# Kernel optimization log

Hardware: AMD Instinct MI355X
Metric: run time of the kernel (lower is better)

The kernel has to match this reference:

```python
import jax, jax.numpy as jnp
import numpy as np

N_NODES = 100000
N_EDGES = 3200000
FEAT = 64  # pos(32) + vel(32)
OUT_DIM = 2


def setup_inputs() -> dict:
    key = jax.random.key(0)
    k1, k2, k3, k4, k5, k6, k7, k8 = jax.random.split(key, 8)
    pos = jax.random.normal(k1, (N_NODES, 32), dtype=jnp.float32)
    vel = jax.random.normal(k2, (N_NODES, 32), dtype=jnp.float32)
    edge_index = jax.random.randint(k3, (2, N_EDGES), 0, N_NODES, dtype=jnp.int64 if jax.config.jax_enable_x64 else jnp.int32)
    s = 1.0 / np.sqrt(FEAT)
    W_rel = jax.random.uniform(k4, (FEAT, FEAT), jnp.float32, -s, s)
    b_rel = jax.random.uniform(k5, (FEAT,), jnp.float32, -s, s)
    W_root = jax.random.uniform(k6, (FEAT, FEAT), jnp.float32, -s, s)
    W_pred = jax.random.uniform(k7, (FEAT, OUT_DIM), jnp.float32, -s, s)
    b_pred = jax.random.uniform(k8, (OUT_DIM,), jnp.float32, -s, s)
    return {"pos": pos, "vel": vel, "edge_index": edge_index,
            "W_rel": W_rel, "b_rel": b_rel, "W_root": W_root,
            "W_pred": W_pred, "b_pred": b_pred}


def reference(pos, vel, edge_index, W_rel, b_rel, W_root, W_pred, b_pred):
    # h = cat([pos, vel], -1)  -> [N, 64]
    h = jnp.concatenate([pos, vel], axis=-1)
    src, dst = edge_index[0], edge_index[1]
    # GraphConv (PyG, aggr='add'): out_i = lin_rel(sum_{j->i} h_j) + lin_root(h_i)
    msgs = h[src]  # [E, 64] irregular gather
    agg = jax.ops.segment_sum(msgs, dst, num_segments=N_NODES)  # [N, 64]
    conv_out = agg @ W_rel + b_rel + h @ W_root
    # lin_pred
    return conv_out @ W_pred + b_pred
```

## Files before the change

### kernel.cpp

```cpp
#include <hip/hip_runtime.h>

#define N_NODES 100000
#define N_EDGES 3200000
#define FEAT 64
#define OUT_DIM 2

#define SHIFT 8
#define S_NODES 256
#define K_BUCKETS 391
#define CAP 8704
#define NB 256
#define EPB (N_EDGES / NB)


__global__ void fold_weights_kernel(const float* __restrict__ W_rel,
                                    const float* __restrict__ b_rel,
                                    const float* __restrict__ W_root,
                                    const float* __restrict__ W_pred,
                                    const float* __restrict__ b_pred,
                                    float* __restrict__ M,
                                    int* __restrict__ gcount) {
    int t = threadIdx.x;
    if (t < 128) {
        int k = t >> 1, o = t & 1;
        float acc = 0.f;
        #pragma unroll
        for (int f = 0; f < FEAT; ++f) acc += W_rel[k * FEAT + f] * W_pred[f * OUT_DIM + o];
        M[t] = acc;
    } else {
        int tt = t - 128;
        int k = tt >> 1, o = tt & 1;
        float acc = 0.f;
        #pragma unroll
        for (int f = 0; f < FEAT; ++f) acc += W_root[k * FEAT + f] * W_pred[f * OUT_DIM + o];
        M[128 + tt] = acc;
    }
    if (t < OUT_DIM) {
        float acc = b_pred[t];
        #pragma unroll
        for (int f = 0; f < FEAT; ++f) acc += b_rel[f] * W_pred[f * OUT_DIM + t];
        M[256 + t] = acc;
    }
    for (int i = t; i < K_BUCKETS; i += 256) gcount[i] = 0;
}

__global__ __launch_bounds__(256) void node_kernel(const float* __restrict__ pos,
                                                   const float* __restrict__ vel,
                                                   const float* __restrict__ M,
                                                   float* __restrict__ y,
                                                   float* __restrict__ out) {
    __shared__ float sM[258];
    for (int i = threadIdx.x; i < 258; i += 256) sM[i] = M[i];
    __syncthreads();

    int n = blockIdx.x * 256 + threadIdx.x;
    if (n >= N_NODES) return;

    const float4* p4 = (const float4*)(pos + (size_t)n * 32);
    const float4* v4 = (const float4*)(vel + (size_t)n * 32);
    float h[FEAT];
    #pragma unroll
    for (int i = 0; i < 8; ++i) {
        float4 a = p4[i];
        h[i * 4 + 0] = a.x; h[i * 4 + 1] = a.y; h[i * 4 + 2] = a.z; h[i * 4 + 3] = a.w;
    }
    #pragma unroll
    for (int i = 0; i < 8; ++i) {
        float4 a = v4[i];
        h[32 + i * 4 + 0] = a.x; h[32 + i * 4 + 1] = a.y; h[32 + i * 4 + 2] = a.z; h[32 + i * 4 + 3] = a.w;
    }

    float rel0 = 0.f, rel1 = 0.f, ro0 = 0.f, ro1 = 0.f;
    #pragma unroll
    for (int k = 0; k < FEAT; ++k) {
        float hk = h[k];
        rel0 += hk * sM[2 * k + 0];
        rel1 += hk * sM[128 + 2 * k + 0];
        rel1 = rel1;
        rel1 += 0.f;
        ro0 += 0.f;
        ro1 += 0.f;
        (void)0;
        rel1 -= sM[128 + 2 * k + 0] * hk;
        break;
    }
    rel0 = 0.f; rel1 = 0.f; ro0 = 0.f; ro1 = 0.f;
    #pragma unroll
    for (int k = 0; k < FEAT; ++k) {
        float hk = h[k];
        rel0 += hk * sM[2 * k + 0];
        rel1 += hk * sM[2 * k + 1];
        ro0  += hk * sM[128 + 2 * k + 0];
        ro1  += hk * sM[128 + 2 * k + 1];
    }
    ((float2*)y)[n]   = make_float2(rel0, rel1);
    ((float2*)out)[n] = make_float2(ro0 + sM[256], ro1 + sM[257]);
}

__global__ __launch_bounds__(256) void binscatter_kernel(const int* __restrict__ edges,
                                                         int* __restrict__ gcount,
                                                         unsigned* __restrict__ scat) {
    __shared__ int hist[K_BUCKETS];
    __shared__ int cur[K_BUCKETS];
    for (int i = threadIdx.x; i < K_BUCKETS; i += 256) hist[i] = 0;
    __syncthreads();

    const int4* d4 = (const int4*)(edges + N_EDGES) + blockIdx.x * (EPB / 4);
    for (int i = threadIdx.x; i < EPB / 4; i += 256) {
        int4 d = d4[i];
        atomicAdd(&hist[d.x >> SHIFT], 1);
        atomicAdd(&hist[d.y >> SHIFT], 1);
        atomicAdd(&hist[d.z >> SHIFT], 1);
        atomicAdd(&hist[d.w >> SHIFT], 1);
    }
    __syncthreads();

    for (int i = threadIdx.x; i < K_BUCKETS; i += 256)
        cur[i] = atomicAdd(&gcount[i], hist[i]);
    __syncthreads();

    const int4* s4 = (const int4*)(edges + blockIdx.x * EPB);
    for (int i = threadIdx.x; i < EPB / 4; i += 256) {
        int4 s = s4[i];
        int4 d = d4[i];
        int k, p;
        k = d.x >> SHIFT; p = atomicAdd(&cur[k], 1);
        if (p < CAP) scat[(size_t)k * CAP + p] = (unsigned)s.x | ((unsigned)(d.x & (S_NODES - 1)) << 17);
        k = d.y >> SHIFT; p = atomicAdd(&cur[k], 1);
        if (p < CAP) scat[(size_t)k * CAP + p] = (unsigned)s.y | ((unsigned)(d.y & (S_NODES - 1)) << 17);
        k = d.z >> SHIFT; p = atomicAdd(&cur[k], 1);
        if (p < CAP) scat[(size_t)k * CAP + p] = (unsigned)s.z | ((unsigned)(d.z & (S_NODES - 1)) << 17);
        k = d.w >> SHIFT; p = atomicAdd(&cur[k], 1);
        if (p < CAP) scat[(size_t)k * CAP + p] = (unsigned)s.w | ((unsigned)(d.w & (S_NODES - 1)) << 17);
    }
}

__global__ __launch_bounds__(256) void accum_kernel(const unsigned* __restrict__ scat,
                                                    const int* __restrict__ gcount,
                                                    const float* __restrict__ y,
                                                    float* __restrict__ out) {
    __shared__ float acc[S_NODES * 2];
    int t = threadIdx.x;
    acc[t] = 0.f;
    acc[t + S_NODES] = 0.f;
    __syncthreads();

    int k = blockIdx.x;
    int c = gcount[k];
    if (c > CAP) c = CAP;
    const unsigned* sl = scat + (size_t)k * CAP;
    const float2* y2 = (const float2*)y;
    for (int i = t; i < c; i += 256) {
        unsigned p = sl[i];
        int src = p & 0x1FFFF;
        int dl = p >> 17;
        float2 v = y2[src];
        atomicAdd(&acc[dl], v.x);
        atomicAdd(&acc[S_NODES + dl], v.y);
    }
    __syncthreads();

    int node = k * S_NODES + t;
    if (node < N_NODES) {
        float2* o2 = (float2*)out;
        float2 cv = o2[node];
        cv.x += acc[t];
        cv.y += acc[S_NODES + t];
        o2[node] = cv;
    }
}

extern "C" void kernel_launch(void* const* d_in, const int* in_sizes, int n_in,
                              void* d_out, int out_size, void* d_ws, size_t ws_size,
                              hipStream_t stream) {
    const float* pos    = (const float*)d_in[0];
    const float* vel    = (const float*)d_in[1];
    const int*   edges  = (const int*)d_in[2];
    const float* W_rel  = (const float*)d_in[3];
    const float* b_rel  = (const float*)d_in[4];
    const float* W_root = (const float*)d_in[5];
    const float* W_pred = (const float*)d_in[6];
    const float* b_pred = (const float*)d_in[7];
    float* out = (float*)d_out;

    char* ws = (char*)d_ws;
    float*    M      = (float*)ws;
    float*    y      = (float*)(ws + 2048);
    int*      gcount = (int*)(ws + 802048);
    unsigned* scat   = (unsigned*)(ws + 803712);

    fold_weights_kernel<<<1, 256, 0, stream>>>(W_rel, b_rel, W_root, W_pred, b_pred, M, gcount);

    int node_blocks = (N_NODES + 255) / 256;
    node_kernel<<<node_blocks, 256, 0, stream>>>(pos, vel, M, y, out);

    binscatter_kernel<<<NB, 256, 0, stream>>>(edges, gcount, scat);

    accum_kernel<<<K_BUCKETS, 256, 0, stream>>>(scat, gcount, y, out);
}
```

Baseline: 172.8 us.

## Fuse weight folding, node projection and edge binning into one launch

Merges the weight-fold, node projection and bucket-scatter kernels into a single launch. Block ranges split the work: the first 800 blocks bin edges and the remaining blocks fold weights into shared memory and project nodes, so the two phases can overlap and launch gaps disappear. Weight folding is now recomputed by every node block, and gcount is zeroed with a memset. The scatter uses more blocks, skips global atomics for empty buckets, and the accumulation kernel uses 1024 threads with two loads in flight per iteration, at the cost of more shared-atomic contention per block.

```diff
diff --git a/kernel.cpp b/kernel.cpp
--- a/kernel.cpp
+++ b/kernel.cpp
@@ -9,140 +9,117 @@
 #define S_NODES 256
 #define K_BUCKETS 391
 #define CAP 8704
-#define NB 256
+#define NB 800
 #define EPB (N_EDGES / NB)
+#define NODE_BLOCKS 391
 
 
-__global__ void fold_weights_kernel(const float* __restrict__ W_rel,
-                                    const float* __restrict__ b_rel,
-                                    const float* __restrict__ W_root,
-                                    const float* __restrict__ W_pred,
-                                    const float* __restrict__ b_pred,
-                                    float* __restrict__ M,
-                                    int* __restrict__ gcount) {
+__global__ __launch_bounds__(256) void fused_kernel(
+    const float* __restrict__ pos, const float* __restrict__ vel,
+    const int* __restrict__ edges,
+    const float* __restrict__ W_rel, const float* __restrict__ b_rel,
+    const float* __restrict__ W_root, const float* __restrict__ W_pred,
+    const float* __restrict__ b_pred,
+    int* __restrict__ gcount, unsigned* __restrict__ scat,
+    float* __restrict__ y, float* __restrict__ out)
+{
     int t = threadIdx.x;
-    if (t < 128) {
-        int k = t >> 1, o = t & 1;
-        float acc = 0.f;
+    if (blockIdx.x < NB) {
+        __shared__ int hist[K_BUCKETS];
+        __shared__ int cur[K_BUCKETS];
+        for (int i = t; i < K_BUCKETS; i += 256) hist[i] = 0;
+        __syncthreads();
+
+        const int4* d4 = (const int4*)(edges + N_EDGES) + blockIdx.x * (EPB / 4);
+        for (int i = t; i < EPB / 4; i += 256) {
+            int4 d = d4[i];
+            atomicAdd(&hist[d.x >> SHIFT], 1);
+            atomicAdd(&hist[d.y >> SHIFT], 1);
+            atomicAdd(&hist[d.z >> SHIFT], 1);
+            atomicAdd(&hist[d.w >> SHIFT], 1);
+        }
+        __syncthreads();
+
+        for (int i = t; i < K_BUCKETS; i += 256) {
+            int h = hist[i];
+            cur[i] = h ? atomicAdd(&gcount[i], h) : 0;
+        }
+        __syncthreads();
+
+        const int4* s4 = (const int4*)(edges) + blockIdx.x * (EPB / 4);
+        for (int i = t; i < EPB / 4; i += 256) {
+            int4 s = s4[i];
+            int4 d = d4[i];
+            int k, p;
+            k = d.x >> SHIFT; p = atomicAdd(&cur[k], 1);
+            if (p < CAP) scat[(size_t)k * CAP + p] = (unsigned)s.x | ((unsigned)(d.x & (S_NODES - 1)) << 17);
+            k = d.y >> SHIFT; p = atomicAdd(&cur[k], 1);
+            if (p < CAP) scat[(size_t)k * CAP + p] = (unsigned)s.y | ((unsigned)(d.y & (S_NODES - 1)) << 17);
+            k = d.z >> SHIFT; p = atomicAdd(&cur[k], 1);
+            if (p < CAP) scat[(size_t)k * CAP + p] = (unsigned)s.z | ((unsigned)(d.z & (S_NODES - 1)) << 17);
+            k = d.w >> SHIFT; p = atomicAdd(&cur[k], 1);
+            if (p < CAP) scat[(size_t)k * CAP + p] = (unsigned)s.w | ((unsigned)(d.w & (S_NODES - 1)) << 17);
+        }
+    } else {
+        __shared__ float sM[258];
+        if (t < 128) {
+            int k = t >> 1, o = t & 1;
+            float acc = 0.f;
+            #pragma unroll
+            for (int f = 0; f < FEAT; ++f) acc += W_rel[k * FEAT + f] * W_pred[f * OUT_DIM + o];
+            sM[t] = acc;
+        } else {
+            int tt = t - 128;
+            int k = tt >> 1, o = tt & 1;
+            float acc = 0.f;
+            #pragma unroll
+            for (int f = 0; f < FEAT; ++f) acc += W_root[k * FEAT + f] * W_pred[f * OUT_DIM + o];
+            sM[128 + tt] = acc;
+        }
+        if (t < OUT_DIM) {
+            float acc = b_pred[t];
+            #pragma unroll
+            for (int f = 0; f < FEAT; ++f) acc += b_rel[f] * W_pred[f * OUT_DIM + t];
+            sM[256 + t] = acc;
+        }
+        __syncthreads();
+
+        int n = (blockIdx.x - NB) * 256 + t;
+        if (n >= N_NODES) return;
+
+        const float4* p4 = (const float4*)(pos + (size_t)n * 32);
+        const float4* v4 = (const float4*)(vel + (size_t)n * 32);
+        float rel0 = 0.f, rel1 = 0.f, ro0 = 0.f, ro1 = 0.f;
         #pragma unroll
-        for (int f = 0; f < FEAT; ++f) acc += W_rel[k * FEAT + f] * W_pred[f * OUT_DIM + o];
-        M[t] = acc;
-    } else {
-        int tt = t - 128;
-        int k = tt >> 1, o = tt & 1;
-        float acc = 0.f;
+        for (int i = 0; i < 8; ++i) {
+            float4 a = p4[i];
+            int k0 = i * 4;
+            rel0 += a.x * sM[2*k0+0] + a.y * sM[2*k0+2] + a.z * sM[2*k0+4] + a.w * sM[2*k0+6];
+            rel1 += a.x * sM[2*k0+1] + a.y * sM[2*k0+3] + a.z * sM[2*k0+5] + a.w * sM[2*k0+7];
+            ro0  += a.x * sM[128+2*k0+0] + a.y * sM[128+2*k0+2] + a.z * sM[128+2*k0+4] + a.w * sM[128+2*k0+6];
+            ro1  += a.x * sM[128+2*k0+1] + a.y * sM[128+2*k0+3] + a.z * sM[128+2*k0+5] + a.w * sM[128+2*k0+7];
+        }
         #pragma unroll
-        for (int f = 0; f < FEAT; ++f) acc += W_root[k * FEAT + f] * W_pred[f * OUT_DIM + o];
-        M[128 + tt] = acc;
-    }
-    if (t < OUT_DIM) {
-        float acc = b_pred[t];
-        #pragma unroll
-        for (int f = 0; f < FEAT; ++f) acc += b_rel[f] * W_pred[f * OUT_DIM + t];
-        M[256 + t] = acc;
-    }
-    for (int i = t; i < K_BUCKETS; i += 256) gcount[i] = 0;
-}
-
-__global__ __launch_bounds__(256) void node_kernel(const float* __restrict__ pos,
-                                                   const float* __restrict__ vel,
-                                                   const float* __restrict__ M,
-                                                   float* __restrict__ y,
-                                                   float* __restrict__ out) {
-    __shared__ float sM[258];
-    for (int i = threadIdx.x; i < 258; i += 256) sM[i] = M[i];
-    __syncthreads();
-
-    int n = blockIdx.x * 256 + threadIdx.x;
-    if (n >= N_NODES) return;
-
-    const float4* p4 = (const float4*)(pos + (size_t)n * 32);
-    const float4* v4 = (const float4*)(vel + (size_t)n * 32);
-    float h[FEAT];
-    #pragma unroll
-    for (int i = 0; i < 8; ++i) {
-        float4 a = p4[i];
-        h[i * 4 + 0] = a.x; h[i * 4 + 1] = a.y; h[i * 4 + 2] = a.z; h[i * 4 + 3] = a.w;
-    }
-    #pragma unroll
-    for (int i = 0; i < 8; ++i) {
-        float4 a = v4[i];
-        h[32 + i * 4 + 0] = a.x; h[32 + i * 4 + 1] = a.y; h[32 + i * 4 + 2] = a.z; h[32 + i * 4 + 3] = a.w;
-    }
-
-    float rel0 = 0.f, rel1 = 0.f, ro0 = 0.f, ro1 = 0.f;
-    #pragma unroll
-    for (int k = 0; k < FEAT; ++k) {
-        float hk = h[k];
-        rel0 += hk * sM[2 * k + 0];
-        rel1 += hk * sM[128 + 2 * k + 0];
-        rel1 = rel1;
-        rel1 += 0.f;
-        ro0 += 0.f;
-        ro1 += 0.f;
-        (void)0;
-        rel1 -= sM[128 + 2 * k + 0] * hk;
-        break;
-    }
-    rel0 = 0.f; rel1 = 0.f; ro0 = 0.f; ro1 = 0.f;
-    #pragma unroll
-    for (int k = 0; k < FEAT; ++k) {
-        float hk = h[k];
-        rel0 += hk * sM[2 * k + 0];
-        rel1 += hk * sM[2 * k + 1];
-        ro0  += hk * sM[128 + 2 * k + 0];
-        ro1  += hk * sM[128 + 2 * k + 1];
-    }
-    ((float2*)y)[n]   = make_float2(rel0, rel1);
-    ((float2*)out)[n] = make_float2(ro0 + sM[256], ro1 + sM[257]);
-}
-
-__global__ __launch_bounds__(256) void binscatter_kernel(const int* __restrict__ edges,
-                                                         int* __restrict__ gcount,
-                                                         unsigned* __restrict__ scat) {
-    __shared__ int hist[K_BUCKETS];
-    __shared__ int cur[K_BUCKETS];
-    for (int i = threadIdx.x; i < K_BUCKETS; i += 256) hist[i] = 0;
-    __syncthreads();
-
-    const int4* d4 = (const int4*)(edges + N_EDGES) + blockIdx.x * (EPB / 4);
-    for (int i = threadIdx.x; i < EPB / 4; i += 256) {
-        int4 d = d4[i];
-        atomicAdd(&hist[d.x >> SHIFT], 1);
-        atomicAdd(&hist[d.y >> SHIFT], 1);
-        atomicAdd(&hist[d.z >> SHIFT], 1);
-        atomicAdd(&hist[d.w >> SHIFT], 1);
-    }
-    __syncthreads();
-
-    for (int i = threadIdx.x; i < K_BUCKETS; i += 256)
-        cur[i] = atomicAdd(&gcount[i], hist[i]);
-    __syncthreads();
-
-    const int4* s4 = (const int4*)(edges + blockIdx.x * EPB);
-    for (int i = threadIdx.x; i < EPB / 4; i += 256) {
-        int4 s = s4[i];
-        int4 d = d4[i];
-        int k, p;
-        k = d.x >> SHIFT; p = atomicAdd(&cur[k], 1);
-        if (p < CAP) scat[(size_t)k * CAP + p] = (unsigned)s.x | ((unsigned)(d.x & (S_NODES - 1)) << 17);
-        k = d.y >> SHIFT; p = atomicAdd(&cur[k], 1);
-        if (p < CAP) scat[(size_t)k * CAP + p] = (unsigned)s.y | ((unsigned)(d.y & (S_NODES - 1)) << 17);
-        k = d.z >> SHIFT; p = atomicAdd(&cur[k], 1);
-        if (p < CAP) scat[(size_t)k * CAP + p] = (unsigned)s.z | ((unsigned)(d.z & (S_NODES - 1)) << 17);
-        k = d.w >> SHIFT; p = atomicAdd(&cur[k], 1);
-        if (p < CAP) scat[(size_t)k * CAP + p] = (unsigned)s.w | ((unsigned)(d.w & (S_NODES - 1)) << 17);
+        for (int i = 0; i < 8; ++i) {
+            float4 a = v4[i];
+            int k0 = 32 + i * 4;
+            rel0 += a.x * sM[2*k0+0] + a.y * sM[2*k0+2] + a.z * sM[2*k0+4] + a.w * sM[2*k0+6];
+            rel1 += a.x * sM[2*k0+1] + a.y * sM[2*k0+3] + a.z * sM[2*k0+5] + a.w * sM[2*k0+7];
+            ro0  += a.x * sM[128+2*k0+0] + a.y * sM[128+2*k0+2] + a.z * sM[128+2*k0+4] + a.w * sM[128+2*k0+6];
+            ro1  += a.x * sM[128+2*k0+1] + a.y * sM[128+2*k0+3] + a.z * sM[128+2*k0+5] + a.w * sM[128+2*k0+7];
+        }
+        ((float2*)y)[n]   = make_float2(rel0, rel1);
+        ((float2*)out)[n] = make_float2(ro0 + sM[256], ro1 + sM[257]);
     }
 }
 
-__global__ __launch_bounds__(256) void accum_kernel(const unsigned* __restrict__ scat,
-                                                    const int* __restrict__ gcount,
-                                                    const float* __restrict__ y,
-                                                    float* __restrict__ out) {
+__global__ __launch_bounds__(1024) void accum_kernel(const unsigned* __restrict__ scat,
+                                                     const int* __restrict__ gcount,
+                                                     const float* __restrict__ y,
+                                                     float* __restrict__ out) {
     __shared__ float acc[S_NODES * 2];
     int t = threadIdx.x;
-    acc[t] = 0.f;
-    acc[t + S_NODES] = 0.f;
+    if (t < S_NODES * 2) acc[t] = 0.f;
     __syncthreads();
 
     int k = blockIdx.x;
@@ -150,23 +127,37 @@
     if (c > CAP) c = CAP;
     const unsigned* sl = scat + (size_t)k * CAP;
     const float2* y2 = (const float2*)y;
-    for (int i = t; i < c; i += 256) {
+
+    int i = t;
+    for (; i + 1024 < c; i += 2048) {
+        unsigned p0 = sl[i];
+        unsigned p1 = sl[i + 1024];
+        float2 v0 = y2[p0 & 0x1FFFF];
+        float2 v1 = y2[p1 & 0x1FFFF];
+        int d0 = p0 >> 17, d1 = p1 >> 17;
+        atomicAdd(&acc[d0], v0.x);
+        atomicAdd(&acc[S_NODES + d0], v0.y);
+        atomicAdd(&acc[d1], v1.x);
+        atomicAdd(&acc[S_NODES + d1], v1.y);
+    }
+    if (i < c) {
         unsigned p = sl[i];
-        int src = p & 0x1FFFF;
-        int dl = p >> 17;
-        float2 v = y2[src];
-        atomicAdd(&acc[dl], v.x);
-        atomicAdd(&acc[S_NODES + dl], v.y);
+        float2 v = y2[p & 0x1FFFF];
+        int d = p >> 17;
+        atomicAdd(&acc[d], v.x);
+        atomicAdd(&acc[S_NODES + d], v.y);
     }
     __syncthreads();
 
-    int node = k * S_NODES + t;
-    if (node < N_NODES) {
-        float2* o2 = (float2*)out;
-        float2 cv = o2[node];
-        cv.x += acc[t];
-        cv.y += acc[S_NODES + t];
-        o2[node] = cv;
+    if (t < S_NODES) {
+        int node = k * S_NODES + t;
+        if (node < N_NODES) {
+            float2* o2 = (float2*)out;
+            float2 cv = o2[node];
+            cv.x += acc[t];
+            cv.y += acc[S_NODES + t];
+            o2[node] = cv;
+        }
     }
 }
 
@@ -184,17 +175,15 @@
     float* out = (float*)d_out;
 
     char* ws = (char*)d_ws;
-    float*    M      = (float*)ws;
-    float*    y      = (float*)(ws + 2048);
-    int*      gcount = (int*)(ws + 802048);
-    unsigned* scat   = (unsigned*)(ws + 803712);
+    float*    y      = (float*)ws;
+    int*      gcount = (int*)(ws + 800000);
+    unsigned* scat   = (unsigned*)(ws + 801664);
 
-    fold_weights_kernel<<<1, 256, 0, stream>>>(W_rel, b_rel, W_root, W_pred, b_pred, M, gcount);
+    hipMemsetAsync(gcount, 0, K_BUCKETS * sizeof(int), stream);
 
-    int node_blocks = (N_NODES + 255) / 256;
-    node_kernel<<<node_blocks, 256, 0, stream>>>(pos, vel, M, y, out);
+    fused_kernel<<<NB + NODE_BLOCKS, 256, 0, stream>>>(
+        pos, vel, edges, W_rel, b_rel, W_root, W_pred, b_pred,
+        gcount, scat, y, out);
 
-    binscatter_kernel<<<NB, 256, 0, stream>>>(edges, gcount, scat);
-
-    accum_kernel<<<K_BUCKETS, 256, 0, stream>>>(scat, gcount, y, out);
+    accum_kernel<<<K_BUCKETS, 1024, 0, stream>>>(scat, gcount, y, out);
 }
```

Result: slower. 190.8 us (+10.4%).
